# Kernel tuning notes

Hardware: AMD Instinct MI355X
Metric: run time of the kernel (lower is better)

Reference implementation:

```python
import jax, jax.numpy as jnp
import numpy as np

H = 4096          # hidden_size
NH = 32           # num query heads
NKV = 8           # num kv heads
HD = H // NH      # head_dim = 128
GROUP = NH // NKV # 4 query heads per kv head
ROPE_BASE = 10000.0
SLIDING_WINDOW = 4096
SCALE = HD ** -0.5


def _rope_interleaved(x, positions):
    # non-neox (GPT-J) style: rotate adjacent pairs (x0,x1),(x2,x3),...
    # x: [B, S, n, HD], positions: [B, S]
    inv_freq = ROPE_BASE ** (-jnp.arange(0, HD, 2, dtype=jnp.float32) / HD)  # [HD/2]
    ang = positions.astype(jnp.float32)[..., None] * inv_freq  # [B, S, HD/2]
    cos = jnp.cos(ang)[:, :, None, :]  # [B, S, 1, HD/2]
    sin = jnp.sin(ang)[:, :, None, :]
    xp = x.reshape(*x.shape[:-1], HD // 2, 2)
    x1, x2 = xp[..., 0], xp[..., 1]
    o1 = x1 * cos - x2 * sin
    o2 = x2 * cos + x1 * sin
    return jnp.stack([o1, o2], axis=-1).reshape(x.shape)


def setup_inputs() -> dict:
    key = jax.random.key(0)
    k1, k2, k3 = jax.random.split(key, 3)
    B, S = 2, 2048
    hidden_states = jax.random.normal(k1, (B, S, H), dtype=jnp.float32)
    positions = jnp.tile(jnp.arange(S, dtype=jnp.int32), (B, 1))
    wqkv = jax.random.normal(k2, (H, NH * HD + 2 * NKV * HD), dtype=jnp.float32) * (H ** -0.5)
    wo = jax.random.normal(k3, (NH * HD, H), dtype=jnp.float32) * ((NH * HD) ** -0.5)
    return {"hidden_states": hidden_states, "positions": positions, "wqkv": wqkv, "wo": wo}


def reference(hidden_states, positions, wqkv, wo):
    B, S, _ = hidden_states.shape
    qkv = hidden_states @ wqkv  # [B, S, 6144]
    q, k, v = jnp.split(qkv, [NH * HD, NH * HD + NKV * HD], axis=-1)
    q = q.reshape(B, S, NH, HD)
    k = k.reshape(B, S, NKV, HD)
    v = v.reshape(B, S, NKV, HD)
    q = _rope_interleaved(q, positions)
    k = _rope_interleaved(k, positions)
    # GQA: group query heads over kv heads
    qg = q.reshape(B, S, NKV, GROUP, HD)
    scores = jnp.einsum('bqkgd,bskd->bkgqs', qg, k) * SCALE  # [B, NKV, GROUP, S, S]
    i = jnp.arange(S)[:, None]
    j = jnp.arange(S)[None, :]
    allowed = (j <= i) & (i - j < SLIDING_WINDOW)  # causal + sliding window
    scores = jnp.where(allowed, scores, jnp.float32(-1e30))
    probs = jax.nn.softmax(scores, axis=-1)
    out = jnp.einsum('bkgqs,bskd->bqkgd', probs, v).reshape(B, S, NH * HD)
    return out @ wo
```

## Files before the change

### kernel.cpp

```cpp
#include <hip/hip_runtime.h>
#include <hip/hip_bf16.h>
#include <stdint.h>

#define Hdim 4096
#define NH 32
#define NKV 8
#define HDs 128
#define Bb 2
#define Ss 2048
#define QKV_N 6144
#define SCALEF 0.08838834764831845f
#define LOG2E 1.4426950408889634f

typedef __attribute__((ext_vector_type(4))) float f32x4;
typedef __attribute__((ext_vector_type(8))) short bf16x8;

__device__ __forceinline__ unsigned short f2bf(float f) {
  union { float f; unsigned u; } v; v.f = f;
  unsigned r = v.u + 0x7fffu + ((v.u >> 16) & 1u);
  return (unsigned short)(r >> 16);
}
__device__ __forceinline__ float bf2f(unsigned short h) {
  union { unsigned u; float f; } v; v.u = ((unsigned)h) << 16;
  return v.f;
}

#define GLOBAL_AS(p) ((const __attribute__((address_space(1))) void*)(p))
#define LDS_AS(p)    ((__attribute__((address_space(3))) void*)(p))

__global__ void k_f32_to_bf16(const float* __restrict__ src, unsigned short* __restrict__ dst, int n) {
  int i = (blockIdx.x * blockDim.x + threadIdx.x) * 4;
  if (i >= n) return;
  f32x4 v = *(const f32x4*)(src + i);
  uint2 o;
  o.x = (unsigned)f2bf(v.x) | ((unsigned)f2bf(v.y) << 16);
  o.y = (unsigned)f2bf(v.z) | ((unsigned)f2bf(v.w) << 16);
  *(uint2*)(dst + i) = o;
}

__global__ void k_transpose_bf16(const float* __restrict__ src, unsigned short* __restrict__ dst,
                                 int K, int N) {
  __shared__ unsigned short tile[32][33];
  int n0 = blockIdx.x * 32, k0 = blockIdx.y * 32;
  int tx = threadIdx.x, ty0 = threadIdx.y;
#pragma unroll
  for (int i = 0; i < 4; i++) {
    int ty = ty0 + i * 8;
    tile[ty][tx] = f2bf(src[(size_t)(k0 + ty) * N + n0 + tx]);
  }
  __syncthreads();
#pragma unroll
  for (int i = 0; i < 4; i++) {
    int ty = ty0 + i * 8;
    dst[(size_t)(n0 + ty) * K + k0 + tx] = tile[tx][ty];
  }
}

template <int OUT_BF16>
__global__ __launch_bounds__(512) void k_gemm8(const unsigned short* __restrict__ A,
                                               const unsigned short* __restrict__ Bt,
                                               void* __restrict__ C,
                                               int M, int N, int K, int nbn) {
  __shared__ __align__(16) unsigned short As[3][256 * 64];
  __shared__ __align__(16) unsigned short Bs[3][128 * 64];

  int nwg = gridDim.x;
  int orig = blockIdx.x;
  int wg = (orig & 7) * (nwg >> 3) + (orig >> 3);
  int bm = wg / nbn, bn = wg % nbn;

  int t = threadIdx.x, w = t >> 6, lane = t & 63;
  int wm = w >> 1, wn = w & 1;
  int l15 = lane & 15, l4 = lane >> 4;

  const unsigned short* Ag = A + (size_t)(bm * 256) * K;
  const unsigned short* Bg = Bt + (size_t)(bn * 128) * K;

  int srow = w * 8 + (lane >> 3);
  int sloff = ((lane & 7) ^ ((lane >> 3) & 7)) * 8;

  f32x4 zero = {0.f, 0.f, 0.f, 0.f};
  f32x4 acc[4][4];
#pragma unroll
  for (int m = 0; m < 4; m++)
#pragma unroll
    for (int n = 0; n < 4; n++) acc[m][n] = zero;

  int NKT = K >> 6;

  auto stage_half = [&](int buf, int kt, int h) {
#pragma unroll
    for (int i2 = 0; i2 < 2; i2++) {
      int row = h * 128 + i2 * 64 + srow;
      __builtin_amdgcn_global_load_lds(GLOBAL_AS(Ag + (size_t)row * K + kt * 64 + sloff),
                                       LDS_AS(&As[buf][h * 8192 + i2 * 4096 + w * 512]), 16, 0, 0);
    }
    {
      int row = h * 64 + srow;
      __builtin_amdgcn_global_load_lds(GLOBAL_AS(Bg + (size_t)row * K + kt * 64 + sloff),
                                       LDS_AS(&Bs[buf][h * 4096 + w * 512]), 16, 0, 0);
    }
  };

  stage_half(0, 0, 0); stage_half(0, 0, 1);
  stage_half(1, 1, 0); stage_half(1, 1, 1);
  asm volatile("s_waitcnt vmcnt(6)" ::: "memory");
  __builtin_amdgcn_s_barrier();

  for (int kt = 0; kt < NKT; kt++) {
    int cb = kt % 3;
    const unsigned short* Abp = As[cb];
    const unsigned short* Bbp = Bs[cb];
#pragma unroll
    for (int q = 0; q < 2; q++) {
      bf16x8 af[4], bf[4];
#pragma unroll
      for (int m = 0; m < 4; m++) {
        int row = wm * 64 + m * 16 + l15;
        int ph = (q * 4 + l4) ^ (row & 7);
        af[m] = *(const bf16x8*)&Abp[row * 64 + ph * 8];
      }
#pragma unroll
      for (int n = 0; n < 4; n++) {
        int row = wn * 64 + n * 16 + l15;
        int ph = (q * 4 + l4) ^ (row & 7);
        bf[n] = *(const bf16x8*)&Bbp[row * 64 + ph * 8];
      }
      if (kt + 2 < NKT) stage_half((kt + 2) % 3, kt + 2, q);
      __builtin_amdgcn_s_barrier();
      asm volatile("s_waitcnt lgkmcnt(0)" ::: "memory");
      __builtin_amdgcn_sched_barrier(0);
      __builtin_amdgcn_s_setprio(1);
#pragma unroll
      for (int m = 0; m < 4; m++)
#pragma unroll
        for (int n = 0; n < 4; n++)
          acc[m][n] = __builtin_amdgcn_mfma_f32_16x16x32_bf16(af[m], bf[n], acc[m][n], 0, 0, 0);
      __builtin_amdgcn_s_setprio(0);
      if (q == 1) {
        if (kt + 2 < NKT) asm volatile("s_waitcnt vmcnt(6)" ::: "memory");
        else              asm volatile("s_waitcnt vmcnt(0)" ::: "memory");
      }
      __builtin_amdgcn_s_barrier();
    }
  }

#pragma unroll
  for (int m = 0; m < 4; m++)
#pragma unroll
    for (int n = 0; n < 4; n++) {
      int col = bn * 128 + wn * 64 + n * 16 + l15;
#pragma unroll
      for (int r = 0; r < 4; r++) {
        int row = bm * 256 + wm * 64 + m * 16 + l4 * 4 + r;
        float v = acc[m][n][r];
        if (OUT_BF16)
          ((unsigned short*)C)[(size_t)row * N + col] = f2bf(v);
        else
          ((float*)C)[(size_t)row * N + col] = v;
      }
    }
}

__global__ void k_rope(unsigned short* __restrict__ qkv, const int* __restrict__ pos) {
  int bs = blockIdx.y;
  int t = threadIdx.x;
  int head = blockIdx.x * 4 + (t >> 6);
  int p = t & 63;
  int col;
  float scale;
  if (head < NH) { col = head * HDs + 2 * p; scale = SCALEF * LOG2E; }
  else           { col = NH * HDs + (head - NH) * HDs + 2 * p; scale = 1.f; }
  size_t idx = (size_t)bs * QKV_N + col;
  float x0 = bf2f(qkv[idx]), x1 = bf2f(qkv[idx + 1]);
  float position = (float)pos[bs];
  float inv_freq = exp2f((float)p * -0.2076205059304601f);
  float ang = position * inv_freq;
  float sv, cv;
  sincosf(ang, &sv, &cv);
  float o0 = (x0 * cv - x1 * sv) * scale;
  float o1 = (x1 * cv + x0 * sv) * scale;
  qkv[idx]     = f2bf(o0);
  qkv[idx + 1] = f2bf(o1);
}

__global__ void k_vt(const unsigned short* __restrict__ qkv, unsigned short* __restrict__ vt) {
  __shared__ unsigned short tile[32][33];
  int bkv = blockIdx.z;
  int d0 = blockIdx.y * 32;
  int s0 = blockIdx.x * 32;
  int b = bkv >> 3, kvh = bkv & 7;
  int tx = threadIdx.x, ty0 = threadIdx.y;
  const unsigned short* src = qkv + (size_t)b * Ss * QKV_N + NH * HDs + NKV * HDs + kvh * HDs;
#pragma unroll
  for (int i = 0; i < 4; i++) {
    int ty = ty0 + i * 8;
    tile[ty][tx] = src[(size_t)(s0 + ty) * QKV_N + d0 + tx];
  }
  __syncthreads();
  unsigned short* dst = vt + (size_t)bkv * HDs * Ss;
#pragma unroll
  for (int i = 0; i < 4; i++) {
    int ty = ty0 + i * 8;
    dst[(size_t)(d0 + ty) * Ss + s0 + tx] = tile[tx][ty];
  }
}

__global__ __launch_bounds__(256, 2) void k_attn(const unsigned short* __restrict__ qkv,
                                                 const unsigned short* __restrict__ vt,
                                                 unsigned short* __restrict__ out) {
  __shared__ __align__(16) unsigned short Ks[2][64 * 128];
  __shared__ __align__(16) unsigned short Vs[2][128 * 64];
  __shared__ __align__(16) unsigned short Ps[4][32 * 64];

  int bid = blockIdx.x;
  int qc = 15 - (bid & 15);
  int h = (bid >> 4) & 31;
  int b = bid >> 9;
  int kvh = h >> 2;
  int t = threadIdx.x;
  int w = t >> 6, lane = t & 63;
  int l15 = lane & 15, l4 = lane >> 4;
  int qb0 = qc * 128;
  int qw = qb0 + w * 32;

  const unsigned short* kbase = qkv + (size_t)b * Ss * QKV_N + NH * HDs + (size_t)kvh * HDs;
  const unsigned short* vbase = vt + ((size_t)(b * NKV + kvh)) * HDs * Ss;

  bf16x8 qf[2][4];
#pragma unroll
  for (int qt = 0; qt < 2; qt++)
#pragma unroll
    for (int ch = 0; ch < 4; ch++)
      qf[qt][ch] = *(const bf16x8*)&qkv[((size_t)(b * Ss) + qw + qt * 16 + l15) * QKV_N +
                                        (size_t)h * HDs + ch * 32 + l4 * 8];

  f32x4 zero = {0.f, 0.f, 0.f, 0.f};
  f32x4 acc[2][8];
#pragma unroll
  for (int qt = 0; qt < 2; qt++)
#pragma unroll
    for (int dt = 0; dt < 8; dt++) acc[qt][dt] = zero;
  float mrun[2] = {-1e30f, -1e30f}, lsum[2] = {0.f, 0.f};

  int nkv = qc * 2 + 2;

  auto stage = [&](int bufi, int kv_) {
#pragma unroll
    for (int r_ = 0; r_ < 4; r_++) {
      int krow = r_ * 16 + w * 4 + (lane >> 4);
      int kls = (lane & 15) ^ (krow & 7);
      __builtin_amdgcn_global_load_lds(GLOBAL_AS(kbase + (size_t)(kv_ + krow) * QKV_N + kls * 8),
                                       LDS_AS(&Ks[bufi][r_ * 2048 + w * 512]), 16, 0, 0);
    }
#pragma unroll
    for (int r_ = 0; r_ < 4; r_++) {
      int vrow = r_ * 32 + w * 8 + (lane >> 3);
      int vls = (lane & 7) ^ (vrow & 7);
      __builtin_amdgcn_global_load_lds(GLOBAL_AS(vbase + (size_t)vrow * Ss + kv_ + vls * 8),
                                       LDS_AS(&Vs[bufi][r_ * 2048 + w * 512]), 16, 0, 0);
    }
  };

  stage(0, 0);
  for (int it = 0; it < nkv; it++) {
    int kvb = it * 64;
    if (it + 1 < nkv) {
      stage((it + 1) & 1, kvb + 64);
      asm volatile("s_waitcnt vmcnt(8)" ::: "memory");
    } else {
      asm volatile("s_waitcnt vmcnt(0)" ::: "memory");
    }
    __builtin_amdgcn_s_barrier();
    if (kvb <= qw + 31) {
      const unsigned short* Kb = Ks[it & 1];
      const unsigned short* Vb = Vs[it & 1];
      unsigned short* Pw = Ps[w];
      bool act0 = (kvb <= qw + 15);

      f32x4 sacc[2][4];
#pragma unroll
      for (int qt = 0; qt < 2; qt++)
#pragma unroll
        for (int kt2 = 0; kt2 < 4; kt2++) sacc[qt][kt2] = zero;
#pragma unroll
      for (int kt2 = 0; kt2 < 4; kt2++) {
        int row = kt2 * 16 + l15;
#pragma unroll
        for (int ch = 0; ch < 4; ch++) {
          int ps = (ch * 4 + l4) ^ (row & 7);
          bf16x8 kf = *(const bf16x8*)&Kb[row * 128 + ps * 8];
          if (act0) sacc[0][kt2] = __builtin_amdgcn_mfma_f32_16x16x32_bf16(kf, qf[0][ch], sacc[0][kt2], 0, 0, 0);
          sacc[1][kt2] = __builtin_amdgcn_mfma_f32_16x16x32_bf16(kf, qf[1][ch], sacc[1][kt2], 0, 0, 0);
        }
      }

#pragma unroll
      for (int qt = 0; qt < 2; qt++) {
        if (qt == 0 && !act0) continue;
        int qi = qw + qt * 16 + l15;
        bool fullvis = (kvb + 63 <= qw + qt * 16);
        float pv[16];
        float tmax = -1e30f;
#pragma unroll
        for (int kt2 = 0; kt2 < 4; kt2++)
#pragma unroll
          for (int r = 0; r < 4; r++) {
            int kvi = kvb + kt2 * 16 + l4 * 4 + r;
            float v = sacc[qt][kt2][r];
            if (!fullvis) v = (kvi <= qi) ? v : -1e30f;
            pv[kt2 * 4 + r] = v;
            tmax = fmaxf(tmax, v);
          }
        tmax = fmaxf(tmax, __shfl_xor(tmax, 16));
        tmax = fmaxf(tmax, __shfl_xor(tmax, 32));
        if (!__all(tmax - mrun[qt] <= 8.f)) {
          float mnew = fmaxf(mrun[qt], tmax);
          float fsc = exp2f(mrun[qt] - mnew);
          mrun[qt] = mnew;
          lsum[qt] *= fsc;
          float fr[4];
#pragma unroll
          for (int r = 0; r < 4; r++) fr[r] = __shfl(fsc, l4 * 4 + r);
#pragma unroll
          for (int dt = 0; dt < 8; dt++)
#pragma unroll
            for (int r = 0; r < 4; r++) acc[qt][dt][r] *= fr[r];
        }
        float rs = 0.f;
#pragma unroll
        for (int i = 0; i < 16; i++) {
          pv[i] = exp2f(pv[i] - mrun[qt]);
          rs += pv[i];
        }
        rs += __shfl_xor(rs, 16);
        rs += __shfl_xor(rs, 32);
        lsum[qt] += rs;
        int prow = qt * 16 + l15;
#pragma unroll
        for (int kt2 = 0; kt2 < 4; kt2++)
#pragma unroll
          for (int rp = 0; rp < 2; rp++) {
            int kv = kt2 * 16 + l4 * 4 + rp * 2;
            int ps = (kv >> 3) ^ (l15 & 7);
            unsigned u = (unsigned)f2bf(pv[kt2 * 4 + rp * 2]) |
                         ((unsigned)f2bf(pv[kt2 * 4 + rp * 2 + 1]) << 16);
            *(unsigned*)&Pw[prow * 64 + ps * 8 + (kv & 7)] = u;
          }
      }

#pragma unroll
      for (int kc = 0; kc < 2; kc++) {
        int psp = (kc * 4 + l4) ^ (l15 & 7);
        bf16x8 pa0 = *(const bf16x8*)&Pw[l15 * 64 + psp * 8];
        bf16x8 pa1 = *(const bf16x8*)&Pw[(16 + l15) * 64 + psp * 8];
#pragma unroll
        for (int dt = 0; dt < 8; dt++) {
          int d = dt * 16 + l15;
          int ps = (kc * 4 + l4) ^ (d & 7);
          bf16x8 vf = *(const bf16x8*)&Vb[d * 64 + ps * 8];
          if (act0) acc[0][dt] = __builtin_amdgcn_mfma_f32_16x16x32_bf16(pa0, vf, acc[0][dt], 0, 0, 0);
          acc[1][dt] = __builtin_amdgcn_mfma_f32_16x16x32_bf16(pa1, vf, acc[1][dt], 0, 0, 0);
        }
      }
    }
    asm volatile("s_waitcnt lgkmcnt(0)" ::: "memory");
    __builtin_amdgcn_s_barrier();
  }

#pragma unroll
  for (int qt = 0; qt < 2; qt++) {
    float lr[4];
#pragma unroll
    for (int r = 0; r < 4; r++) lr[r] = __shfl(lsum[qt], l4 * 4 + r);
#pragma unroll
    for (int dt = 0; dt < 8; dt++)
#pragma unroll
      for (int r = 0; r < 4; r++) {
        int row = qw + qt * 16 + l4 * 4 + r;
        out[((size_t)(b * Ss) + row) * Hdim + (size_t)h * HDs + dt * 16 + l15] =
            f2bf(acc[qt][dt][r] / lr[r]);
      }
  }
}

extern "C" void kernel_launch(void* const* d_in, const int* in_sizes, int n_in,
                              void* d_out, int out_size, void* d_ws, size_t ws_size,
                              hipStream_t stream) {
  const float* hidden = (const float*)d_in[0];
  const int* positions = (const int*)d_in[1];
  const float* wqkv = (const float*)d_in[2];
  const float* wo = (const float*)d_in[3];
  float* out = (float*)d_out;
  char* ws = (char*)d_ws;

  unsigned short* hbf  = (unsigned short*)(ws);
  unsigned short* wT   = (unsigned short*)(ws + 33554432);
  unsigned short* qkvb = (unsigned short*)(ws + 83886080);
  unsigned short* vtb  = (unsigned short*)(ws + 134217728);

  k_f32_to_bf16<<<16384, 256, 0, stream>>>(hidden, hbf, Bb * Ss * Hdim);
  k_transpose_bf16<<<dim3(QKV_N / 32, Hdim / 32), dim3(32, 8), 0, stream>>>(wqkv, wT, Hdim, QKV_N);
  k_gemm8<1><<<(4096 / 256) * (QKV_N / 128), 512, 0, stream>>>(hbf, wT, qkvb, 4096, QKV_N, 4096, QKV_N / 128);
  k_rope<<<dim3(10, Bb * Ss), 256, 0, stream>>>(qkvb, positions);
  k_vt<<<dim3(Ss / 32, HDs / 32, Bb * NKV), dim3(32, 8), 0, stream>>>(qkvb, vtb);
  k_transpose_bf16<<<dim3(Hdim / 32, Hdim / 32), dim3(32, 8), 0, stream>>>(wo, wT, Hdim, Hdim);
  k_attn<<<Bb * NH * (Ss / 128), 256, 0, stream>>>(qkvb, vtb, hbf);
  k_gemm8<0><<<(4096 / 256) * (4096 / 128), 512, 0, stream>>>(hbf, wT, out, 4096, 4096, 4096, 4096 / 128);
}
```

Measured before the change: 702.7 us.

## Keep softmax probabilities in registers via permuted V layout, single-buffer V

The V transpose now writes columns in a permuted order within each 64-wide block. That lets the bf16-packed probability registers from the QK MFMA output feed the PV MFMA directly, so the per-warp LDS round trip for P goes away. V is single-buffered and loaded at the start of each iteration, with a second barrier and a vmcnt wait before the PV stage. This cuts LDS use and raises launch bounds to 3 blocks per SM. The cost is an extra barrier and V load latency sitting on the critical path. Probability packing now uses the v_cvt_pk_bf16_f32 instruction.

```diff
diff --git a/kernel.cpp b/kernel.cpp
--- a/kernel.cpp
+++ b/kernel.cpp
@@ -23,6 +23,11 @@
 __device__ __forceinline__ float bf2f(unsigned short h) {
   union { unsigned u; float f; } v; v.u = ((unsigned)h) << 16;
   return v.f;
+}
+__device__ __forceinline__ unsigned cvtpk(float lo, float hi) {
+  unsigned r;
+  asm("v_cvt_pk_bf16_f32 %0, %1, %2" : "=v"(r) : "v"(lo), "v"(hi));
+  return r;
 }
 
 #define GLOBAL_AS(p) ((const __attribute__((address_space(1))) void*)(p))
@@ -199,19 +204,21 @@
   }
   __syncthreads();
   unsigned short* dst = vt + (size_t)bkv * HDs * Ss;
+  int c = s0 + tx;
+  int o = c & 63;
+  int pcol = (c & ~63) | ((o & 32) | ((o & 12) << 1) | ((o & 16) >> 2) | (o & 3));
 #pragma unroll
   for (int i = 0; i < 4; i++) {
     int ty = ty0 + i * 8;
-    dst[(size_t)(d0 + ty) * Ss + s0 + tx] = tile[tx][ty];
-  }
-}
-
-__global__ __launch_bounds__(256, 2) void k_attn(const unsigned short* __restrict__ qkv,
+    dst[(size_t)(d0 + ty) * Ss + pcol] = tile[tx][ty];
+  }
+}
+
+__global__ __launch_bounds__(256, 3) void k_attn(const unsigned short* __restrict__ qkv,
                                                  const unsigned short* __restrict__ vt,
                                                  unsigned short* __restrict__ out) {
   __shared__ __align__(16) unsigned short Ks[2][64 * 128];
-  __shared__ __align__(16) unsigned short Vs[2][128 * 64];
-  __shared__ __align__(16) unsigned short Ps[4][32 * 64];
+  __shared__ __align__(16) unsigned short Vs[128 * 64];
 
   int bid = blockIdx.x;
   int qc = 15 - (bid & 15);
@@ -245,7 +252,7 @@
 
   int nkv = qc * 2 + 2;
 
-  auto stage = [&](int bufi, int kv_) {
+  auto stageK = [&](int bufi, int kv_) {
 #pragma unroll
     for (int r_ = 0; r_ < 4; r_++) {
       int krow = r_ * 16 + w * 4 + (lane >> 4);
@@ -253,31 +260,33 @@
       __builtin_amdgcn_global_load_lds(GLOBAL_AS(kbase + (size_t)(kv_ + krow) * QKV_N + kls * 8),
                                        LDS_AS(&Ks[bufi][r_ * 2048 + w * 512]), 16, 0, 0);
     }
+  };
+  auto stageV = [&](int kv_) {
 #pragma unroll
     for (int r_ = 0; r_ < 4; r_++) {
       int vrow = r_ * 32 + w * 8 + (lane >> 3);
       int vls = (lane & 7) ^ (vrow & 7);
       __builtin_amdgcn_global_load_lds(GLOBAL_AS(vbase + (size_t)vrow * Ss + kv_ + vls * 8),
-                                       LDS_AS(&Vs[bufi][r_ * 2048 + w * 512]), 16, 0, 0);
+                                       LDS_AS(&Vs[r_ * 2048 + w * 512]), 16, 0, 0);
     }
   };
 
-  stage(0, 0);
+  stageK(0, 0);
   for (int it = 0; it < nkv; it++) {
     int kvb = it * 64;
-    if (it + 1 < nkv) {
-      stage((it + 1) & 1, kvb + 64);
-      asm volatile("s_waitcnt vmcnt(8)" ::: "memory");
-    } else {
-      asm volatile("s_waitcnt vmcnt(0)" ::: "memory");
-    }
+    bool more = (it + 1 < nkv);
+    stageV(kvb);
+    if (more) stageK((it + 1) & 1, kvb + 64);
+    if (more) asm volatile("s_waitcnt vmcnt(8)" ::: "memory");
+    else      asm volatile("s_waitcnt vmcnt(4)" ::: "memory");
     __builtin_amdgcn_s_barrier();
-    if (kvb <= qw + 31) {
+
+    bool active = (kvb <= qw + 31);
+    bool act0 = (kvb <= qw + 15);
+    bf16x8 pa[2][2];
+
+    if (active) {
       const unsigned short* Kb = Ks[it & 1];
-      const unsigned short* Vb = Vs[it & 1];
-      unsigned short* Pw = Ps[w];
-      bool act0 = (kvb <= qw + 15);
-
       f32x4 sacc[2][4];
 #pragma unroll
       for (int qt = 0; qt < 2; qt++)
@@ -336,35 +345,33 @@
         rs += __shfl_xor(rs, 16);
         rs += __shfl_xor(rs, 32);
         lsum[qt] += rs;
-        int prow = qt * 16 + l15;
-#pragma unroll
-        for (int kt2 = 0; kt2 < 4; kt2++)
-#pragma unroll
-          for (int rp = 0; rp < 2; rp++) {
-            int kv = kt2 * 16 + l4 * 4 + rp * 2;
-            int ps = (kv >> 3) ^ (l15 & 7);
-            unsigned u = (unsigned)f2bf(pv[kt2 * 4 + rp * 2]) |
-                         ((unsigned)f2bf(pv[kt2 * 4 + rp * 2 + 1]) << 16);
-            *(unsigned*)&Pw[prow * 64 + ps * 8 + (kv & 7)] = u;
-          }
-      }
-
+        union { unsigned u[4]; bf16x8 v8; } pk0, pk1;
+#pragma unroll
+        for (int i = 0; i < 4; i++) pk0.u[i] = cvtpk(pv[2 * i], pv[2 * i + 1]);
+#pragma unroll
+        for (int i = 0; i < 4; i++) pk1.u[i] = cvtpk(pv[8 + 2 * i], pv[8 + 2 * i + 1]);
+        pa[qt][0] = pk0.v8;
+        pa[qt][1] = pk1.v8;
+      }
+    }
+
+    if (more) asm volatile("s_waitcnt vmcnt(4)" ::: "memory");
+    else      asm volatile("s_waitcnt vmcnt(0)" ::: "memory");
+    __builtin_amdgcn_s_barrier();
+
+    if (active) {
 #pragma unroll
       for (int kc = 0; kc < 2; kc++) {
-        int psp = (kc * 4 + l4) ^ (l15 & 7);
-        bf16x8 pa0 = *(const bf16x8*)&Pw[l15 * 64 + psp * 8];
-        bf16x8 pa1 = *(const bf16x8*)&Pw[(16 + l15) * 64 + psp * 8];
 #pragma unroll
         for (int dt = 0; dt < 8; dt++) {
           int d = dt * 16 + l15;
           int ps = (kc * 4 + l4) ^ (d & 7);
-          bf16x8 vf = *(const bf16x8*)&Vb[d * 64 + ps * 8];
-          if (act0) acc[0][dt] = __builtin_amdgcn_mfma_f32_16x16x32_bf16(pa0, vf, acc[0][dt], 0, 0, 0);
-          acc[1][dt] = __builtin_amdgcn_mfma_f32_16x16x32_bf16(pa1, vf, acc[1][dt], 0, 0, 0);
+          bf16x8 vf = *(const bf16x8*)&Vs[d * 64 + ps * 8];
+          if (act0) acc[0][dt] = __builtin_amdgcn_mfma_f32_16x16x32_bf16(pa[0][kc], vf, acc[0][dt], 0, 0, 0);
+          acc[1][dt] = __builtin_amdgcn_mfma_f32_16x16x32_bf16(pa[1][kc], vf, acc[1][dt], 0, 0, 0);
         }
       }
     }
-    asm volatile("s_waitcnt lgkmcnt(0)" ::: "memory");
     __builtin_amdgcn_s_barrier();
   }
 
```

Result: slower. 1.015 ms (+44.5%).
